# Kernel tuning notes

Hardware: AMD Instinct MI355X
Metric: run time of the kernel (lower is better)

Reference implementation:

```python
import jax, jax.numpy as jnp
import numpy as np

NUM_HEADS = 32
HEAD_SIZE = 80
ROT_DIM = 32
HIDDEN = NUM_HEADS * HEAD_SIZE  # 2560
LN_EPS = 1e-5


def setup_inputs() -> dict:
    key = jax.random.key(0)
    ks = jax.random.split(key, 11)
    B, S, H = 2, 2048, HIDDEN
    s = 1.0 / np.sqrt(H)
    return {
        "hidden_states": jax.random.normal(ks[0], (B, S, H), jnp.float32),
        "ln_weight": jax.random.uniform(ks[1], (H,), jnp.float32, 0.5, 1.5),
        "ln_bias": jax.random.normal(ks[2], (H,), jnp.float32) * 0.02,
        "qkv_weight": jax.random.normal(ks[3], (H, 3 * H), jnp.float32) * s,
        "qkv_bias": jax.random.normal(ks[4], (3 * H,), jnp.float32) * 0.02,
        "out_weight": jax.random.normal(ks[5], (H, H), jnp.float32) * s,
        "out_bias": jax.random.normal(ks[6], (H,), jnp.float32) * 0.02,
        "fc1_weight": jax.random.normal(ks[7], (H, 4 * H), jnp.float32) * s,
        "fc1_bias": jax.random.normal(ks[8], (4 * H,), jnp.float32) * 0.02,
        "fc2_weight": jax.random.normal(ks[9], (4 * H, H), jnp.float32) * (1.0 / np.sqrt(4 * H)),
        "fc2_bias": jax.random.normal(ks[10], (H,), jnp.float32) * 0.02,
    }


def _layernorm(x, w, b):
    mu = jnp.mean(x, axis=-1, keepdims=True)
    var = jnp.mean(jnp.square(x - mu), axis=-1, keepdims=True)
    return (x - mu) * jax.lax.rsqrt(var + LN_EPS) * w + b


def _fast_gelu(x):
    # ONNX FastGelu: tanh approximation
    c = np.sqrt(2.0 / np.pi).astype(np.float32)
    return 0.5 * x * (1.0 + jnp.tanh(c * (x + 0.044715 * x * x * x)))


def _apply_partial_rope(x, cos, sin):
    # x: [B,S,nh,hd]; rotate first ROT_DIM dims, non-interleaved (half split)
    half = ROT_DIM // 2
    x1 = x[..., :half]
    x2 = x[..., half:ROT_DIM]
    rot1 = x1 * cos - x2 * sin
    rot2 = x1 * sin + x2 * cos
    return jnp.concatenate([rot1, rot2, x[..., ROT_DIM:]], axis=-1)


def reference(hidden_states, ln_weight, ln_bias, qkv_weight, qkv_bias,
              out_weight, out_bias, fc1_weight, fc1_bias, fc2_weight, fc2_bias):
    B, S, H = hidden_states.shape
    ln_out = _layernorm(hidden_states, ln_weight, ln_bias)

    # fused QKV
    qkv = ln_out @ qkv_weight + qkv_bias  # [B,S,3H]
    q, k, v = jnp.split(qkv, 3, axis=-1)
    q = q.reshape(B, S, NUM_HEADS, HEAD_SIZE)
    k = k.reshape(B, S, NUM_HEADS, HEAD_SIZE)
    v = v.reshape(B, S, NUM_HEADS, HEAD_SIZE)

    # partial rotary embeddings
    half = ROT_DIM // 2
    inv_freq = 1.0 / (10000.0 ** (jnp.arange(0, half, dtype=jnp.float32) * 2.0 / ROT_DIM))
    pos = jnp.arange(S, dtype=jnp.float32)
    angles = pos[:, None] * inv_freq[None, :]          # [S, half]
    cos = jnp.cos(angles)[None, :, None, :]           # [1,S,1,half]
    sin = jnp.sin(angles)[None, :, None, :]
    q = _apply_partial_rope(q, cos, sin)
    k = _apply_partial_rope(k, cos, sin)

    # causal attention
    scale = 1.0 / np.sqrt(HEAD_SIZE).astype(np.float32)
    scores = jnp.einsum('bqhd,bkhd->bhqk', q, k) * scale
    causal = jnp.tril(jnp.ones((S, S), dtype=bool))
    scores = jnp.where(causal[None, None], scores, jnp.finfo(scores.dtype).min)
    probs = jax.nn.softmax(scores, axis=-1)
    attn = jnp.einsum('bhqk,bkhd->bqhd', probs, v).reshape(B, S, H)
    attn_out = attn @ out_weight + out_bias

    # MLP on same LN output (parallel block)
    mlp = _fast_gelu(ln_out @ fc1_weight + fc1_bias) @ fc2_weight + fc2_bias

    return hidden_states + attn_out + mlp
```

## Files before the change

### kernel.cpp

```cpp
#include <hip/hip_runtime.h>
#include <cstdint>

#define NUM_HEADS 32
#define HEAD 80
#define DQK 104
#define HID 2560
#define H3 7680
#define H4 10240
#define BB 2
#define SS 2048
#define ROWS (BB*SS)

typedef __bf16 bf16_t;
typedef __bf16 bf16x8 __attribute__((ext_vector_type(8)));
typedef __bf16 bf16x4 __attribute__((ext_vector_type(4)));
typedef float  f32x4  __attribute__((ext_vector_type(4)));

typedef __attribute__((address_space(1))) void* gptr_t;
typedef __attribute__((address_space(3))) void* lptr_t;

__device__ __forceinline__ void async_copy16(const void* g, void* l) {
  __builtin_amdgcn_global_load_lds((gptr_t)g, (lptr_t)l, 16, 0, 0);
}

__global__ __launch_bounds__(256) void wconv(const float* __restrict__ W,
                                             bf16_t* __restrict__ Wt,
                                             int K, int N) {
  __shared__ float tile[32][33];
  const int n0 = blockIdx.x * 32, k0 = blockIdx.y * 32;
  const int tx = threadIdx.x & 31, ty = threadIdx.x >> 5;
#pragma unroll
  for (int i = 0; i < 32; i += 8)
    tile[ty + i][tx] = W[(size_t)(k0 + ty + i) * N + n0 + tx];
  __syncthreads();
#pragma unroll
  for (int i = 0; i < 32; i += 8)
    Wt[(size_t)(n0 + ty + i) * K + k0 + tx] = (bf16_t)tile[tx][ty + i];
}

__global__ __launch_bounds__(256) void ln_kernel(const float* __restrict__ x,
                                                 const float* __restrict__ w,
                                                 const float* __restrict__ b,
                                                 bf16_t* __restrict__ o) {
  const int row = blockIdx.x;
  const int tid = threadIdx.x;
  const int wid = tid >> 6, lane = tid & 63;
  const float4* xr = (const float4*)(x + (size_t)row * HID);
  __shared__ float red[8];

  float4 vals[3];
  int nc = 0;
  float s = 0.f;
  for (int c = tid; c < HID / 4; c += 256) {
    float4 v = xr[c];
    vals[nc++] = v;
    s += v.x + v.y + v.z + v.w;
  }
#pragma unroll
  for (int o2 = 32; o2 > 0; o2 >>= 1) s += __shfl_down(s, o2);
  if (lane == 0) red[wid] = s;
  __syncthreads();
  const float mean = (red[0] + red[1] + red[2] + red[3]) * (1.f / HID);

  float s2 = 0.f;
  nc = 0;
  for (int c = tid; c < HID / 4; c += 256) {
    float4 v = vals[nc++];
    float a0 = v.x - mean, a1 = v.y - mean, a2 = v.z - mean, a3 = v.w - mean;
    s2 += a0 * a0 + a1 * a1 + a2 * a2 + a3 * a3;
  }
#pragma unroll
  for (int o2 = 32; o2 > 0; o2 >>= 1) s2 += __shfl_down(s2, o2);
  __syncthreads();
  if (lane == 0) red[4 + wid] = s2;
  __syncthreads();
  const float var = (red[4] + red[5] + red[6] + red[7]) * (1.f / HID);
  const float rstd = rsqrtf(var + 1e-5f);

  bf16_t* orow = o + (size_t)row * HID;
  nc = 0;
  for (int c = tid; c < HID / 4; c += 256) {
    float4 v = vals[nc++];
    float4 wv = ((const float4*)w)[c];
    float4 bv = ((const float4*)b)[c];
    bf16x4 r4;
    r4[0] = (bf16_t)((v.x - mean) * rstd * wv.x + bv.x);
    r4[1] = (bf16_t)((v.y - mean) * rstd * wv.y + bv.y);
    r4[2] = (bf16_t)((v.z - mean) * rstd * wv.z + bv.z);
    r4[3] = (bf16_t)((v.w - mean) * rstd * wv.w + bv.w);
    *(bf16x4*)(orow + c * 4) = r4;
  }
}

template <int MODE>
__global__ __launch_bounds__(256, 2) void gemm_bt(
    const bf16_t* __restrict__ A, const bf16_t* __restrict__ Bt,
    int M, int N, int K,
    const float* __restrict__ bias,
    float* __restrict__ outF, bf16_t* __restrict__ outB,
    bf16_t* __restrict__ qp, bf16_t* __restrict__ kp, bf16_t* __restrict__ vp,
    const float* __restrict__ add1, const float* __restrict__ add2,
    const float* __restrict__ bias2) {
  __shared__ bf16_t Ash[128 * 32];
  __shared__ bf16_t Bsh[128 * 32];
  const int tid = threadIdx.x;
  const int wid = tid >> 6, lane = tid & 63;
  const int wrow = wid >> 1, wcol = wid & 1;
  const int lr = lane & 15, lq = lane >> 4;
  const int m0 = blockIdx.y * 128;
  const int n0 = blockIdx.x * 128;
  const bf16_t* Ab = A + (size_t)m0 * K;
  const bf16_t* Bb = Bt + (size_t)n0 * K;
  const int srow = wid * 16 + (lane >> 2);
  const int sk = (lane & 3) * 8;

  f32x4 acc[4][4] = {};

  for (int kt = 0; kt < K; kt += 32) {
    __syncthreads();
    async_copy16(Ab + (size_t)srow * K + kt + sk, &Ash[srow * 32 + sk]);
    async_copy16(Ab + (size_t)(srow + 64) * K + kt + sk, &Ash[(srow + 64) * 32 + sk]);
    async_copy16(Bb + (size_t)srow * K + kt + sk, &Bsh[srow * 32 + sk]);
    async_copy16(Bb + (size_t)(srow + 64) * K + kt + sk, &Bsh[(srow + 64) * 32 + sk]);
    __syncthreads();
    bf16x8 af[4], bfr[4];
#pragma unroll
    for (int mi = 0; mi < 4; mi++)
      af[mi] = *(const bf16x8*)&Ash[(wrow * 64 + mi * 16 + lr) * 32 + lq * 8];
#pragma unroll
    for (int ni = 0; ni < 4; ni++)
      bfr[ni] = *(const bf16x8*)&Bsh[(wcol * 64 + ni * 16 + lr) * 32 + lq * 8];
#pragma unroll
    for (int mi = 0; mi < 4; mi++)
#pragma unroll
      for (int ni = 0; ni < 4; ni++)
        acc[mi][ni] = __builtin_amdgcn_mfma_f32_16x16x32_bf16(af[mi], bfr[ni], acc[mi][ni], 0, 0, 0);
  }

  if constexpr (MODE == 0) {
#pragma unroll
    for (int ni = 0; ni < 4; ni++) {
      const int n = n0 + wcol * 64 + ni * 16 + lr;
      const float bn = bias[n];
      const int which = n / HID;
      const int wi = n - which * HID;
      const int hh = wi / HEAD;
      const int dd = wi - hh * HEAD;
#pragma unroll
      for (int mi = 0; mi < 4; mi++) {
#pragma unroll
        for (int r = 0; r < 4; r++) {
          const int m = m0 + wrow * 64 + mi * 16 + lq * 4 + r;
          const int bb2 = m >> 11, ss2 = m & (SS - 1);
          const size_t bh = (size_t)(bb2 * NUM_HEADS + hh);
          float v = acc[mi][ni][r] + bn;
          if (which == 0) {
            qp[(bh * SS + ss2) * DQK + dd] = (bf16_t)(v * 0.16129822f);
          } else if (which == 1) {
            kp[(bh * SS + ss2) * DQK + dd] = (bf16_t)v;
          } else {
            vp[(bh * SS + ss2) * HEAD + dd] = (bf16_t)v;
          }
        }
      }
    }
  } else {
#pragma unroll
    for (int mi = 0; mi < 4; mi++) {
#pragma unroll
      for (int ni = 0; ni < 4; ni++) {
        const int n = n0 + wcol * 64 + ni * 16 + lr;
#pragma unroll
        for (int r = 0; r < 4; r++) {
          const int m = m0 + wrow * 64 + mi * 16 + lq * 4 + r;
          float v = acc[mi][ni][r];
          if constexpr (MODE == 1) {
            v += bias[n];
            const float y = 0.7978845608f * (v + 0.044715f * v * v * v);
            const float a = fabsf(y);
            const float e = exp2f(-2.885390082f * a);
            float t = (1.f - e) * __builtin_amdgcn_rcpf(1.f + e);
            t = copysignf(t, y);
            outB[(size_t)m * N + n] = (bf16_t)(0.5f * v * (1.f + t));
          } else if constexpr (MODE == 2) {
            outF[(size_t)m * N + n] = v;
          } else {
            const size_t idx = (size_t)m * N + n;
            outF[idx] = v + add1[idx] + add2[idx] + bias[n] + bias2[n];
          }
        }
      }
    }
  }
}

__global__ __launch_bounds__(256) void rope_kernel(bf16_t* __restrict__ qp,
                                                   bf16_t* __restrict__ kp) {
  const int idx = blockIdx.x * 256 + threadIdx.x;
  const int d = idx & 15;
  const int bhs = (idx >> 4) & (BB * NUM_HEADS * SS - 1);
  const int isk = idx >> 21;
  bf16_t* base = (isk ? kp : qp) + (size_t)bhs * DQK;
  const int s = bhs & (SS - 1);
  const float fr = exp2f((float)d * -0.830482024f);
  const float ang = (float)s * fr;
  float sn, cs;
  sincosf(ang, &sn, &cs);
  const float x1 = (float)base[d];
  const float x2 = (float)base[d + 16];
  base[d] = (bf16_t)(x1 * cs - x2 * sn);
  base[d + 16] = (bf16_t)(x1 * sn + x2 * cs);
}

__global__ __launch_bounds__(256) void vtrans(const bf16_t* __restrict__ vtmp,
                                              bf16_t* __restrict__ vt) {
  __shared__ bf16_t t[80][72];
  const int tid = threadIdx.x;
  const int bh = blockIdx.z * NUM_HEADS + blockIdx.y;
  const int s0 = blockIdx.x * 64;
  const bf16_t* src = vtmp + ((size_t)bh * SS + s0) * HEAD;
#pragma unroll
  for (int i = 0; i < 5; i++) {
    const int e4 = i * 256 + tid;
    const int row = e4 / 20;
    const int c4 = (e4 % 20) * 4;
    bf16x4 v = *(const bf16x4*)(src + (size_t)row * HEAD + c4);
    t[c4 + 0][row] = v[0];
    t[c4 + 1][row] = v[1];
    t[c4 + 2][row] = v[2];
    t[c4 + 3][row] = v[3];
  }
  __syncthreads();
  bf16_t* dst = vt + (size_t)bh * HEAD * SS + s0;
#pragma unroll
  for (int i = 0; i < 2; i++) {
    const int o = i * 256 + tid;
    const int d = o >> 3, p = o & 7;
    *(bf16x8*)(dst + (size_t)d * SS + p * 8) = *(const bf16x8*)&t[d][(p ^ (d & 7)) * 8];
  }
  if (tid < 128) {
    const int o = 512 + tid;
    const int d = o >> 3, p = o & 7;
    *(bf16x8*)(dst + (size_t)d * SS + p * 8) = *(const bf16x8*)&t[d][(p ^ (d & 7)) * 8];
  }
}

__global__ __launch_bounds__(256, 3) void attn_kernel(
    const bf16_t* __restrict__ qb, const bf16_t* __restrict__ kb,
    const bf16_t* __restrict__ vt, bf16_t* __restrict__ attnb) {
  __shared__ bf16_t Qs[64 * DQK];
  __shared__ bf16_t Ks[64 * DQK];
  __shared__ bf16_t Vs[80 * 64];
  __shared__ bf16_t Ps[4][16 * 72];

  const int tid = threadIdx.x;
  const int wid = tid >> 6, lane = tid & 63;
  const int lr = lane & 15, lq = lane >> 4;
  const int b = blockIdx.z, h = blockIdx.y;
  const int qt = (int)gridDim.x - 1 - (int)blockIdx.x;
  const int q0 = qt * 64;
  const size_t hoff = (size_t)(b * NUM_HEADS + h) * SS;
  const bf16_t* Qg = qb + hoff * DQK + (size_t)q0 * DQK;
  const bf16_t* Kg = kb + hoff * DQK;
  const bf16_t* Vg = vt + hoff * HEAD;

#pragma unroll
  for (int i = 0; i < 3; i++) {
    const int cc = i * 256 + tid;
    async_copy16(Qg + cc * 8, &Qs[cc * 8]);
  }
  if (tid < 64) {
    const int cc = 768 + tid;
    async_copy16(Qg + cc * 8, &Qs[cc * 8]);
  }

  f32x4 oacc[5] = {};
  float lsum[4] = {0.f, 0.f, 0.f, 0.f};
  const int row_base = q0 + wid * 16 + lq * 4;
  const int nkt = qt + 1;

  for (int kt = 0; kt < nkt; kt++) {
    const int k0 = kt * 64;
    __syncthreads();
#pragma unroll
    for (int i = 0; i < 3; i++) {
      const int cc = i * 256 + tid;
      async_copy16(Kg + (size_t)k0 * DQK + cc * 8, &Ks[cc * 8]);
    }
    if (tid < 64) {
      const int cc = 768 + tid;
      async_copy16(Kg + (size_t)k0 * DQK + cc * 8, &Ks[cc * 8]);
    }
#pragma unroll
    for (int i = 0; i < 2; i++) {
      const int c = i * 256 + tid;
      const int d = c >> 3, p = c & 7;
      async_copy16(Vg + (size_t)d * SS + k0 + p * 8, &Vs[c * 8]);
    }
    if (tid < 128) {
      const int c = 512 + tid;
      const int d = c >> 3, p = c & 7;
      async_copy16(Vg + (size_t)d * SS + k0 + p * 8, &Vs[c * 8]);
    }
    __syncthreads();

    f32x4 sacc[4] = {};
#pragma unroll
    for (int kk = 0; kk < 3; kk++) {
      bf16x8 af = *(const bf16x8*)&Qs[(wid * 16 + lr) * DQK + kk * 32 + lq * 8];
#pragma unroll
      for (int ni = 0; ni < 4; ni++) {
        bf16x8 bfr = *(const bf16x8*)&Ks[(ni * 16 + lr) * DQK + kk * 32 + lq * 8];
        sacc[ni] = __builtin_amdgcn_mfma_f32_16x16x32_bf16(af, bfr, sacc[ni], 0, 0, 0);
      }
    }

    const bool last = (kt == nkt - 1);
#pragma unroll
    for (int r = 0; r < 4; r++) {
#pragma unroll
      for (int ni = 0; ni < 4; ni++) {
        float p = exp2f(sacc[ni][r]);
        if (last && (k0 + ni * 16 + lr) > (row_base + r)) p = 0.f;
        lsum[r] += p;
        Ps[wid][(lq * 4 + r) * 72 + ni * 16 + lr] = (bf16_t)p;
      }
    }
    __builtin_amdgcn_s_waitcnt(0xc07f);

#pragma unroll
    for (int kk = 0; kk < 2; kk++) {
      bf16x8 pf = *(const bf16x8*)&Ps[wid][lr * 72 + kk * 32 + lq * 8];
#pragma unroll
      for (int di = 0; di < 5; di++) {
        const int d = di * 16 + lr;
        bf16x8 vf = *(const bf16x8*)&Vs[d * 64 + (((kk * 4 + lq) ^ (d & 7)) * 8)];
        oacc[di] = __builtin_amdgcn_mfma_f32_16x16x32_bf16(pf, vf, oacc[di], 0, 0, 0);
      }
    }
  }

#pragma unroll
  for (int r = 0; r < 4; r++) {
    float l = lsum[r];
    l += __shfl_xor(l, 1);
    l += __shfl_xor(l, 2);
    l += __shfl_xor(l, 4);
    l += __shfl_xor(l, 8);
    const float inv = 1.f / l;
    const int rowg = row_base + r;
    bf16_t* orow = attnb + (size_t)(b * SS + rowg) * HID + h * HEAD;
#pragma unroll
    for (int di = 0; di < 5; di++)
      orow[di * 16 + lr] = (bf16_t)(oacc[di][r] * inv);
  }
}

extern "C" void kernel_launch(void* const* d_in, const int* in_sizes, int n_in,
                              void* d_out, int out_size, void* d_ws, size_t ws_size,
                              hipStream_t stream) {
  const float* hid  = (const float*)d_in[0];
  const float* lnw  = (const float*)d_in[1];
  const float* lnb  = (const float*)d_in[2];
  const float* qkvw = (const float*)d_in[3];
  const float* qkvb = (const float*)d_in[4];
  const float* outw = (const float*)d_in[5];
  const float* outb = (const float*)d_in[6];
  const float* fc1w = (const float*)d_in[7];
  const float* fc1b = (const float*)d_in[8];
  const float* fc2w = (const float*)d_in[9];
  const float* fc2b = (const float*)d_in[10];
  float* out = (float*)d_out;

  char* ws = (char*)d_ws;
  size_t off = 0;
  auto alloc = [&](size_t bytes) -> char* {
    char* p = ws + off;
    off += (bytes + 255) & ~(size_t)255;
    return p;
  };
  bf16_t* qkv_wt = (bf16_t*)alloc((size_t)H3 * HID * 2);
  bf16_t* out_wt = (bf16_t*)alloc((size_t)HID * HID * 2);
  bf16_t* fc1_wt = (bf16_t*)alloc((size_t)H4 * HID * 2);
  bf16_t* fc2_wt = (bf16_t*)alloc((size_t)HID * H4 * 2);
  bf16_t* ln_out = (bf16_t*)alloc((size_t)ROWS * HID * 2);
  bf16_t* q_pad  = (bf16_t*)alloc((size_t)BB * NUM_HEADS * SS * DQK * 2);
  bf16_t* k_pad  = (bf16_t*)alloc((size_t)BB * NUM_HEADS * SS * DQK * 2);
  bf16_t* v_t    = (bf16_t*)alloc((size_t)BB * NUM_HEADS * HEAD * SS * 2);
  bf16_t* attnb  = (bf16_t*)alloc((size_t)ROWS * HID * 2);
  bf16_t* fc1a   = (bf16_t*)alloc((size_t)ROWS * H4 * 2);
  bf16_t* v_tmp = attnb;
  float* aproj = (float*)q_pad;

  wconv<<<dim3(H3 / 32, HID / 32), 256, 0, stream>>>(qkvw, qkv_wt, HID, H3);
  wconv<<<dim3(HID / 32, HID / 32), 256, 0, stream>>>(outw, out_wt, HID, HID);
  wconv<<<dim3(H4 / 32, HID / 32), 256, 0, stream>>>(fc1w, fc1_wt, HID, H4);
  wconv<<<dim3(HID / 32, H4 / 32), 256, 0, stream>>>(fc2w, fc2_wt, H4, HID);

  ln_kernel<<<ROWS, 256, 0, stream>>>(hid, lnw, lnb, ln_out);

  hipMemsetAsync(q_pad, 0, (size_t)BB * NUM_HEADS * SS * DQK * 2, stream);
  hipMemsetAsync(k_pad, 0, (size_t)BB * NUM_HEADS * SS * DQK * 2, stream);

  gemm_bt<0><<<dim3(H3 / 128, ROWS / 128), 256, 0, stream>>>(
      ln_out, qkv_wt, ROWS, H3, HID, qkvb, nullptr, nullptr,
      q_pad, k_pad, v_tmp, nullptr, nullptr, nullptr);

  rope_kernel<<<(BB * NUM_HEADS * SS * 16 * 2) / 256, 256, 0, stream>>>(q_pad, k_pad);

  vtrans<<<dim3(SS / 64, NUM_HEADS, BB), 256, 0, stream>>>(v_tmp, v_t);

  attn_kernel<<<dim3(SS / 64, NUM_HEADS, BB), 256, 0, stream>>>(q_pad, k_pad, v_t, attnb);

  gemm_bt<2><<<dim3(HID / 128, ROWS / 128), 256, 0, stream>>>(
      attnb, out_wt, ROWS, HID, HID, nullptr, aproj, nullptr,
      nullptr, nullptr, nullptr, nullptr, nullptr, nullptr);

  gemm_bt<1><<<dim3(H4 / 128, ROWS / 128), 256, 0, stream>>>(
      ln_out, fc1_wt, ROWS, H4, HID, fc1b, nullptr, fc1a,
      nullptr, nullptr, nullptr, nullptr, nullptr, nullptr);

  gemm_bt<3><<<dim3(HID / 128, ROWS / 128), 256, 0, stream>>>(
      fc1a, fc2_wt, ROWS, HID, H4, fc2b, out, nullptr,
      nullptr, nullptr, nullptr, hid, aproj, outb);
}
```

Baseline: 1.452 ms.

## Concatenate QKV+FC1 and out-proj+FC2 GEMMs, fuse V transpose into epilogue

The QKV and FC1 weights are packed into one transposed matrix so a single GEMM produces q/k/v and the GELU activations. The out-projection and FC2 are merged into one GEMM along K: attention output and GELU activations share a row buffer and the weights are stacked. The separate V transpose kernel is removed by writing V directly in the swizzled transposed layout from the GEMM epilogue. The weight conversion now uses 64x64 vectorized tiles, the GEMM block order is remapped to be M-major, and the occupancy hint in launch bounds is dropped. This cuts kernel launches and the fp32 aproj round trip, at the cost of scattered V stores and possible register or occupancy changes.

```diff
diff --git a/kernel.cpp b/kernel.cpp
--- a/kernel.cpp
+++ b/kernel.cpp
@@ -7,6 +7,8 @@
 #define HID 2560
 #define H3 7680
 #define H4 10240
+#define NA 17920
+#define KB 12800
 #define BB 2
 #define SS 2048
 #define ROWS (BB*SS)
@@ -23,19 +25,30 @@
   __builtin_amdgcn_global_load_lds((gptr_t)g, (lptr_t)l, 16, 0, 0);
 }
 
-__global__ __launch_bounds__(256) void wconv(const float* __restrict__ W,
-                                             bf16_t* __restrict__ Wt,
-                                             int K, int N) {
-  __shared__ float tile[32][33];
-  const int n0 = blockIdx.x * 32, k0 = blockIdx.y * 32;
-  const int tx = threadIdx.x & 31, ty = threadIdx.x >> 5;
-#pragma unroll
-  for (int i = 0; i < 32; i += 8)
-    tile[ty + i][tx] = W[(size_t)(k0 + ty + i) * N + n0 + tx];
+__global__ __launch_bounds__(256) void wconv64(const float* __restrict__ W,
+                                               bf16_t* __restrict__ Wt,
+                                               int K, int N, int ldt) {
+  __shared__ float t[64][65];
+  const int n0 = blockIdx.x * 64, k0 = blockIdx.y * 64;
+  const int tx = threadIdx.x & 15, ty = threadIdx.x >> 4;
+#pragma unroll
+  for (int i = 0; i < 4; i++) {
+    const int row = ty + 16 * i;
+    float4 v = *(const float4*)(W + (size_t)(k0 + row) * N + n0 + tx * 4);
+    t[row][tx * 4 + 0] = v.x;
+    t[row][tx * 4 + 1] = v.y;
+    t[row][tx * 4 + 2] = v.z;
+    t[row][tx * 4 + 3] = v.w;
+  }
   __syncthreads();
 #pragma unroll
-  for (int i = 0; i < 32; i += 8)
-    Wt[(size_t)(n0 + ty + i) * K + k0 + tx] = (bf16_t)tile[tx][ty + i];
+  for (int i = 0; i < 4; i++) {
+    const int n = ty + 16 * i;
+    bf16x4 o;
+#pragma unroll
+    for (int j = 0; j < 4; j++) o[j] = (bf16_t)t[tx * 4 + j][n];
+    *(bf16x4*)(Wt + (size_t)(n0 + n) * ldt + k0 + tx * 4) = o;
+  }
 }
 
 __global__ __launch_bounds__(256) void ln_kernel(const float* __restrict__ x,
@@ -93,22 +106,23 @@
 }
 
 template <int MODE>
-__global__ __launch_bounds__(256, 2) void gemm_bt(
+__global__ __launch_bounds__(256) void gemm_bt(
     const bf16_t* __restrict__ A, const bf16_t* __restrict__ Bt,
     int M, int N, int K,
-    const float* __restrict__ bias,
-    float* __restrict__ outF, bf16_t* __restrict__ outB,
-    bf16_t* __restrict__ qp, bf16_t* __restrict__ kp, bf16_t* __restrict__ vp,
-    const float* __restrict__ add1, const float* __restrict__ add2,
-    const float* __restrict__ bias2) {
+    const float* __restrict__ b0, const float* __restrict__ b1,
+    const float* __restrict__ hid, float* __restrict__ outF,
+    bf16_t* __restrict__ U,
+    bf16_t* __restrict__ qp, bf16_t* __restrict__ kp, bf16_t* __restrict__ vt) {
   __shared__ bf16_t Ash[128 * 32];
   __shared__ bf16_t Bsh[128 * 32];
   const int tid = threadIdx.x;
   const int wid = tid >> 6, lane = tid & 63;
   const int wrow = wid >> 1, wcol = wid & 1;
   const int lr = lane & 15, lq = lane >> 4;
-  const int m0 = blockIdx.y * 128;
-  const int n0 = blockIdx.x * 128;
+  const int Mb = M >> 7;
+  const int bid = blockIdx.x + blockIdx.y * gridDim.x;
+  const int m0 = (bid % Mb) * 128;
+  const int n0 = (bid / Mb) * 128;
   const bf16_t* Ab = A + (size_t)m0 * K;
   const bf16_t* Bb = Bt + (size_t)n0 * K;
   const int srow = wid * 16 + (lane >> 2);
@@ -138,56 +152,69 @@
   }
 
   if constexpr (MODE == 0) {
-#pragma unroll
-    for (int ni = 0; ni < 4; ni++) {
-      const int n = n0 + wcol * 64 + ni * 16 + lr;
-      const float bn = bias[n];
-      const int which = n / HID;
-      const int wi = n - which * HID;
-      const int hh = wi / HEAD;
-      const int dd = wi - hh * HEAD;
-#pragma unroll
-      for (int mi = 0; mi < 4; mi++) {
-#pragma unroll
-        for (int r = 0; r < 4; r++) {
-          const int m = m0 + wrow * 64 + mi * 16 + lq * 4 + r;
-          const int bb2 = m >> 11, ss2 = m & (SS - 1);
-          const size_t bh = (size_t)(bb2 * NUM_HEADS + hh);
-          float v = acc[mi][ni][r] + bn;
-          if (which == 0) {
-            qp[(bh * SS + ss2) * DQK + dd] = (bf16_t)(v * 0.16129822f);
-          } else if (which == 1) {
-            kp[(bh * SS + ss2) * DQK + dd] = (bf16_t)v;
-          } else {
-            vp[(bh * SS + ss2) * HEAD + dd] = (bf16_t)v;
+    if (n0 < H3) {
+#pragma unroll
+      for (int ni = 0; ni < 4; ni++) {
+        const int n = n0 + wcol * 64 + ni * 16 + lr;
+        const float bn = b0[n];
+        const int which = n / HID;
+        const int wi = n - which * HID;
+        const int hh = wi / HEAD;
+        const int dd = wi - hh * HEAD;
+#pragma unroll
+        for (int mi = 0; mi < 4; mi++) {
+#pragma unroll
+          for (int r = 0; r < 4; r++) {
+            const int m = m0 + wrow * 64 + mi * 16 + lq * 4 + r;
+            const int bb2 = m >> 11, ss2 = m & (SS - 1);
+            const size_t bh = (size_t)(bb2 * NUM_HEADS + hh);
+            float v = acc[mi][ni][r] + bn;
+            if (which == 0) {
+              qp[(bh * SS + ss2) * DQK + dd] = (bf16_t)(v * 0.16129822f);
+            } else if (which == 1) {
+              kp[(bh * SS + ss2) * DQK + dd] = (bf16_t)v;
+            } else {
+              const int sblk = ss2 & ~63;
+              const int pch = ((ss2 >> 3) & 7) ^ (dd & 7);
+              vt[(bh * HEAD + dd) * SS + sblk + pch * 8 + (ss2 & 7)] = (bf16_t)v;
+            }
           }
         }
       }
-    }
-  } else {
-#pragma unroll
-    for (int mi = 0; mi < 4; mi++) {
+    } else {
 #pragma unroll
       for (int ni = 0; ni < 4; ni++) {
         const int n = n0 + wcol * 64 + ni * 16 + lr;
-#pragma unroll
-        for (int r = 0; r < 4; r++) {
-          const int m = m0 + wrow * 64 + mi * 16 + lq * 4 + r;
-          float v = acc[mi][ni][r];
-          if constexpr (MODE == 1) {
-            v += bias[n];
+        const int j = n - H3;
+        const float bn = b1[j];
+#pragma unroll
+        for (int mi = 0; mi < 4; mi++) {
+#pragma unroll
+          for (int r = 0; r < 4; r++) {
+            const int m = m0 + wrow * 64 + mi * 16 + lq * 4 + r;
+            float v = acc[mi][ni][r] + bn;
             const float y = 0.7978845608f * (v + 0.044715f * v * v * v);
             const float a = fabsf(y);
             const float e = exp2f(-2.885390082f * a);
             float t = (1.f - e) * __builtin_amdgcn_rcpf(1.f + e);
             t = copysignf(t, y);
-            outB[(size_t)m * N + n] = (bf16_t)(0.5f * v * (1.f + t));
-          } else if constexpr (MODE == 2) {
-            outF[(size_t)m * N + n] = v;
-          } else {
-            const size_t idx = (size_t)m * N + n;
-            outF[idx] = v + add1[idx] + add2[idx] + bias[n] + bias2[n];
+            U[(size_t)m * KB + HID + j] = (bf16_t)(0.5f * v * (1.f + t));
           }
+        }
+      }
+    }
+  } else {
+#pragma unroll
+    for (int mi = 0; mi < 4; mi++) {
+#pragma unroll
+      for (int ni = 0; ni < 4; ni++) {
+        const int n = n0 + wcol * 64 + ni * 16 + lr;
+        const float bn = b0[n] + b1[n];
+#pragma unroll
+        for (int r = 0; r < 4; r++) {
+          const int m = m0 + wrow * 64 + mi * 16 + lq * 4 + r;
+          const size_t idx = (size_t)m * N + n;
+          outF[idx] = acc[mi][ni][r] + hid[idx] + bn;
         }
       }
     }
@@ -212,42 +239,9 @@
   base[d + 16] = (bf16_t)(x1 * sn + x2 * cs);
 }
 
-__global__ __launch_bounds__(256) void vtrans(const bf16_t* __restrict__ vtmp,
-                                              bf16_t* __restrict__ vt) {
-  __shared__ bf16_t t[80][72];
-  const int tid = threadIdx.x;
-  const int bh = blockIdx.z * NUM_HEADS + blockIdx.y;
-  const int s0 = blockIdx.x * 64;
-  const bf16_t* src = vtmp + ((size_t)bh * SS + s0) * HEAD;
-#pragma unroll
-  for (int i = 0; i < 5; i++) {
-    const int e4 = i * 256 + tid;
-    const int row = e4 / 20;
-    const int c4 = (e4 % 20) * 4;
-    bf16x4 v = *(const bf16x4*)(src + (size_t)row * HEAD + c4);
-    t[c4 + 0][row] = v[0];
-    t[c4 + 1][row] = v[1];
-    t[c4 + 2][row] = v[2];
-    t[c4 + 3][row] = v[3];
-  }
-  __syncthreads();
-  bf16_t* dst = vt + (size_t)bh * HEAD * SS + s0;
-#pragma unroll
-  for (int i = 0; i < 2; i++) {
-    const int o = i * 256 + tid;
-    const int d = o >> 3, p = o & 7;
-    *(bf16x8*)(dst + (size_t)d * SS + p * 8) = *(const bf16x8*)&t[d][(p ^ (d & 7)) * 8];
-  }
-  if (tid < 128) {
-    const int o = 512 + tid;
-    const int d = o >> 3, p = o & 7;
-    *(bf16x8*)(dst + (size_t)d * SS + p * 8) = *(const bf16x8*)&t[d][(p ^ (d & 7)) * 8];
-  }
-}
-
 __global__ __launch_bounds__(256, 3) void attn_kernel(
     const bf16_t* __restrict__ qb, const bf16_t* __restrict__ kb,
-    const bf16_t* __restrict__ vt, bf16_t* __restrict__ attnb) {
+    const bf16_t* __restrict__ vt, bf16_t* __restrict__ U) {
   __shared__ bf16_t Qs[64 * DQK];
   __shared__ bf16_t Ks[64 * DQK];
   __shared__ bf16_t Vs[80 * 64];
@@ -349,7 +343,7 @@
     l += __shfl_xor(l, 8);
     const float inv = 1.f / l;
     const int rowg = row_base + r;
-    bf16_t* orow = attnb + (size_t)(b * SS + rowg) * HID + h * HEAD;
+    bf16_t* orow = U + (size_t)(b * SS + rowg) * KB + h * HEAD;
 #pragma unroll
     for (int di = 0; di < 5; di++)
       orow[di * 16 + lr] = (bf16_t)(oacc[di][r] * inv);
@@ -379,48 +373,33 @@
     off += (bytes + 255) & ~(size_t)255;
     return p;
   };
-  bf16_t* qkv_wt = (bf16_t*)alloc((size_t)H3 * HID * 2);
-  bf16_t* out_wt = (bf16_t*)alloc((size_t)HID * HID * 2);
-  bf16_t* fc1_wt = (bf16_t*)alloc((size_t)H4 * HID * 2);
-  bf16_t* fc2_wt = (bf16_t*)alloc((size_t)HID * H4 * 2);
-  bf16_t* ln_out = (bf16_t*)alloc((size_t)ROWS * HID * 2);
-  bf16_t* q_pad  = (bf16_t*)alloc((size_t)BB * NUM_HEADS * SS * DQK * 2);
-  bf16_t* k_pad  = (bf16_t*)alloc((size_t)BB * NUM_HEADS * SS * DQK * 2);
-  bf16_t* v_t    = (bf16_t*)alloc((size_t)BB * NUM_HEADS * HEAD * SS * 2);
-  bf16_t* attnb  = (bf16_t*)alloc((size_t)ROWS * HID * 2);
-  bf16_t* fc1a   = (bf16_t*)alloc((size_t)ROWS * H4 * 2);
-  bf16_t* v_tmp = attnb;
-  float* aproj = (float*)q_pad;
-
-  wconv<<<dim3(H3 / 32, HID / 32), 256, 0, stream>>>(qkvw, qkv_wt, HID, H3);
-  wconv<<<dim3(HID / 32, HID / 32), 256, 0, stream>>>(outw, out_wt, HID, HID);
-  wconv<<<dim3(H4 / 32, HID / 32), 256, 0, stream>>>(fc1w, fc1_wt, HID, H4);
-  wconv<<<dim3(HID / 32, H4 / 32), 256, 0, stream>>>(fc2w, fc2_wt, H4, HID);
+  bf16_t* w1t   = (bf16_t*)alloc((size_t)NA * HID * 2);
+  bf16_t* w2t   = (bf16_t*)alloc((size_t)HID * KB * 2);
+  bf16_t* ln_out= (bf16_t*)alloc((size_t)ROWS * HID * 2);
+  bf16_t* Ubuf  = (bf16_t*)alloc((size_t)ROWS * KB * 2);
+  bf16_t* q_pad = (bf16_t*)alloc((size_t)BB * NUM_HEADS * SS * DQK * 2);
+  bf16_t* k_pad = (bf16_t*)alloc((size_t)BB * NUM_HEADS * SS * DQK * 2);
+  bf16_t* v_t   = (bf16_t*)alloc((size_t)BB * NUM_HEADS * HEAD * SS * 2);
+
+  wconv64<<<dim3(H3 / 64, HID / 64), 256, 0, stream>>>(qkvw, w1t, HID, H3, HID);
+  wconv64<<<dim3(H4 / 64, HID / 64), 256, 0, stream>>>(fc1w, w1t + (size_t)H3 * HID, HID, H4, HID);
+  wconv64<<<dim3(HID / 64, HID / 64), 256, 0, stream>>>(outw, w2t, HID, HID, KB);
+  wconv64<<<dim3(HID / 64, H4 / 64), 256, 0, stream>>>(fc2w, w2t + HID, H4, HID, KB);
 
   ln_kernel<<<ROWS, 256, 0, stream>>>(hid, lnw, lnb, ln_out);
 
   hipMemsetAsync(q_pad, 0, (size_t)BB * NUM_HEADS * SS * DQK * 2, stream);
   hipMemsetAsync(k_pad, 0, (size_t)BB * NUM_HEADS * SS * DQK * 2, stream);
 
-  gemm_bt<0><<<dim3(H3 / 128, ROWS / 128), 256, 0, stream>>>(
-      ln_out, qkv_wt, ROWS, H3, HID, qkvb, nullptr, nullptr,
-      q_pad, k_pad, v_tmp, nullptr, nullptr, nullptr);
+  gemm_bt<0><<<dim3(NA / 128, ROWS / 128), 256, 0, stream>>>(
+      ln_out, w1t, ROWS, NA, HID, qkvb, fc1b,
+      nullptr, nullptr, Ubuf, q_pad, k_pad, v_t);
 
   rope_kernel<<<(BB * NUM_HEADS * SS * 16 * 2) / 256, 256, 0, stream>>>(q_pad, k_pad);
 
-  vtrans<<<dim3(SS / 64, NUM_HEADS, BB), 256, 0, stream>>>(v_tmp, v_t);
-
-  attn_kernel<<<dim3(SS / 64, NUM_HEADS, BB), 256, 0, stream>>>(q_pad, k_pad, v_t, attnb);
-
-  gemm_bt<2><<<dim3(HID / 128, ROWS / 128), 256, 0, stream>>>(
-      attnb, out_wt, ROWS, HID, HID, nullptr, aproj, nullptr,
-      nullptr, nullptr, nullptr, nullptr, nullptr, nullptr);
-
-  gemm_bt<1><<<dim3(H4 / 128, ROWS / 128), 256, 0, stream>>>(
-      ln_out, fc1_wt, ROWS, H4, HID, fc1b, nullptr, fc1a,
-      nullptr, nullptr, nullptr, nullptr, nullptr, nullptr);
-
-  gemm_bt<3><<<dim3(HID / 128, ROWS / 128), 256, 0, stream>>>(
-      fc1a, fc2_wt, ROWS, HID, H4, fc2b, out, nullptr,
-      nullptr, nullptr, nullptr, hid, aproj, outb);
-}
+  attn_kernel<<<dim3(SS / 64, NUM_HEADS, BB), 256, 0, stream>>>(q_pad, k_pad, v_t, Ubuf);
+
+  gemm_bt<1><<<dim3(HID / 128, ROWS / 128), 256, 0, stream>>>(
+      Ubuf, w2t, ROWS, HID, KB, outb, fc2b,
+      hid, out, nullptr, nullptr, nullptr, nullptr);
+}
```

Measured after the change: 1.906 ms. 1.31x slower.
